# Kernel tuning notes

Hardware: AMD Instinct MI355X
Metric: run time of the kernel (lower is better)

The kernel has to match this reference:

```python
import jax, jax.numpy as jnp
import numpy as np

C_IN, K_R, K_C, N_K = 32, 3, 3, 64
STRIDE = (1, 1)
PAD = (1, 1)


def setup_inputs() -> dict:
    key = jax.random.key(0)
    k1, k2, k3 = jax.random.split(key, 3)
    x = jax.random.normal(k1, (32, C_IN, 128, 128), dtype=jnp.float32)
    kernels = jax.random.normal(k2, (N_K, K_R * K_C * C_IN), dtype=jnp.float32) * 0.05
    bias = jax.random.normal(k3, (N_K, 1), dtype=jnp.float32) * 0.05
    return {"x": x, "kernels": kernels, "bias": bias}


def reference(x, kernels, bias):
    # kernels rows are [C, kr, kc] flattened (per-channel im2col blocks stacked
    # along dim 0 in the original unroll) -> OIHW conv weight.
    w = kernels.reshape(N_K, C_IN, K_R, K_C)
    out = jax.lax.conv_general_dilated(
        x, w,
        window_strides=STRIDE,
        padding=[(PAD[0], PAD[0]), (PAD[1], PAD[1])],
        dimension_numbers=("NCHW", "OIHW", "NCHW"),
    )
    # bias (K, 1) broadcast over all output positions
    return out + bias.reshape(1, N_K, 1, 1)
```

## Files before the change

### kernel.cpp

```cpp
#include <hip/hip_runtime.h>
#include <hip/hip_bf16.h>


typedef __attribute__((ext_vector_type(8))) short bf16x8;
typedef __attribute__((ext_vector_type(4))) float f32x4;

#define NB 32
#define CIN 32
#define HH 128
#define WW 128
#define NK 64
#define XROW (130 * 32)

__device__ __forceinline__ unsigned short f2bf(float f) {
    union { float f; unsigned int u; } v; v.f = f;
    unsigned int u = v.u;
    return (unsigned short)((u + 0x7FFFu + ((u >> 16) & 1u)) >> 16);
}

__device__ __forceinline__ int xel(int wi, int c) {
    return wi * 32 + ((((c >> 3) ^ ((wi >> 2) & 3)) << 3) | (c & 7));
}

__global__ void repack_w(const float* __restrict__ kern,
                         unsigned short* __restrict__ wfrag) {
    int u = blockIdx.x * 256 + threadIdx.x;
    int j = u & 7;
    int lane = (u >> 3) & 63;
    int tile = (u >> 9) & 3;
    int kidx = u >> 11;
    int ok = tile * 16 + (lane & 15);
    int c = ((lane >> 4) << 3) + j;
    wfrag[u] = f2bf(kern[ok * 288 + c * 9 + kidx]);
}

__global__ __launch_bounds__(512, 6) void conv3x3_mfma(
        const float* __restrict__ x, const unsigned short* __restrict__ wfrag,
        const float* __restrict__ bias, float* __restrict__ out) {
    __shared__ unsigned short lds_x[4 * XROW];

    const int tid = threadIdx.x;
    const int bx = blockIdx.x;
    const int hp = ((bx & 7) << 3) | (bx >> 3);
    const int h0 = hp * 2;
    const int n = blockIdx.y;
    const int lane = tid & 63;
    const int l16 = lane & 15;
    const int q = lane >> 4;
    const int wav = tid >> 6;
    const int hsel = wav >> 2;
    const int sub = wav & 3;
    const int ok_tile = (sub & 1) * 2;
    const int w_base = (sub >> 1) * 64;

    if (tid < 256) {
        int it = tid >> 6;
        int idx = tid & 63;
        int c = idx & 31;
        int wi = (idx < 32) ? 0 : 129;
        lds_x[it * XROW + xel(wi, c)] = 0;
    }

    {
        const int c = (tid >> 5) * 2;
        const int wq = tid & 31;
        #pragma unroll
        for (int it = 0; it < 4; ++it) {
            const int r = h0 - 1 + it;
            const bool valid = (unsigned)r < HH;
            float4 va = {0.f, 0.f, 0.f, 0.f}, vb = {0.f, 0.f, 0.f, 0.f};
            if (valid) {
                const float* xrow = x + (((size_t)n * CIN + c) * HH + r) * WW;
                va = *((const float4*)xrow + wq);
                vb = *((const float4*)(xrow + (size_t)HH * WW) + wq);
            }
            unsigned short* lrow = lds_x + it * XROW;
            #pragma unroll
            for (int j = 0; j < 4; ++j) {
                int w = wq * 4 + j;
                __hip_bfloat162 h2 = __float22bfloat162_rn(
                    make_float2((&va.x)[j], (&vb.x)[j]));
                *(unsigned int*)&lrow[xel(w + 1, c)] = *(unsigned int*)&h2;
            }
        }
    }
    __syncthreads();

    f32x4 acc[2][4];
    #pragma unroll
    for (int mi = 0; mi < 2; ++mi)
        #pragma unroll
        for (int ni = 0; ni < 4; ++ni)
            acc[mi][ni] = (f32x4){0.f, 0.f, 0.f, 0.f};

    #pragma unroll 1
    for (int kr = 0; kr < 3; ++kr) {
        const unsigned short* lrow = lds_x + (hsel + kr) * XROW;
        #pragma unroll
        for (int kc = 0; kc < 3; ++kc) {
            const int kidx = kr * 3 + kc;
            bf16x8 afr[2];
            #pragma unroll
            for (int mi = 0; mi < 2; ++mi)
                afr[mi] = *(const bf16x8*)
                    &wfrag[(size_t)(((kidx * 4) + ok_tile + mi) * 64 + lane) * 8];
            #pragma unroll
            for (int ni = 0; ni < 4; ++ni) {
                bf16x8 bfr = *(const bf16x8*)&lrow[xel(w_base + ni * 16 + l16 + kc, q * 8)];
                #pragma unroll
                for (int mi = 0; mi < 2; ++mi)
                    acc[mi][ni] = __builtin_amdgcn_mfma_f32_16x16x32_bf16(
                        afr[mi], bfr, acc[mi][ni], 0, 0, 0);
            }
        }
    }

    const int h = h0 + hsel;
    #pragma unroll
    for (int mi = 0; mi < 2; ++mi) {
        #pragma unroll
        for (int rg = 0; rg < 4; ++rg) {
            int ok = (sub & 1) * 32 + mi * 16 + q * 4 + rg;
            float bv = bias[ok];
            float* orow = out + (((size_t)n * NK + ok) * HH + h) * WW;
            #pragma unroll
            for (int ni = 0; ni < 4; ++ni)
                orow[w_base + ni * 16 + l16] = acc[mi][ni][rg] + bv;
        }
    }
}

extern "C" void kernel_launch(void* const* d_in, const int* in_sizes, int n_in,
                              void* d_out, int out_size, void* d_ws, size_t ws_size,
                              hipStream_t stream) {
    const float* x    = (const float*)d_in[0];
    const float* kern = (const float*)d_in[1];
    const float* bias = (const float*)d_in[2];
    float* out = (float*)d_out;
    unsigned short* wfrag = (unsigned short*)d_ws;

    repack_w<<<72, 256, 0, stream>>>(kern, wfrag);
    dim3 grid(64, NB);
    conv3x3_mfma<<<grid, 512, 0, stream>>>(x, wfrag, bias, out);
}
```

Baseline: 199.6 us.

## Process four output rows per block and prefetch the extra input rows during compute

Each block now produces four output rows in two passes instead of two, with a grid half as large. This reuses the halo rows already staged in LDS and cuts redundant input loads. The two extra input rows are loaded into registers before the first pass and written to LDS afterwards, so their global latency overlaps the first pass's MFMA work. LDS use rises to six rows and the occupancy hint drops to 4, so fewer blocks may be resident.

```diff
diff --git a/kernel.cpp b/kernel.cpp
--- a/kernel.cpp
+++ b/kernel.cpp
@@ -34,15 +34,15 @@
     wfrag[u] = f2bf(kern[ok * 288 + c * 9 + kidx]);
 }
 
-__global__ __launch_bounds__(512, 6) void conv3x3_mfma(
+__global__ __launch_bounds__(512, 4) void conv3x3_mfma(
         const float* __restrict__ x, const unsigned short* __restrict__ wfrag,
         const float* __restrict__ bias, float* __restrict__ out) {
-    __shared__ unsigned short lds_x[4 * XROW];
+    __shared__ unsigned short lds_x[6 * XROW];
 
     const int tid = threadIdx.x;
     const int bx = blockIdx.x;
-    const int hp = ((bx & 7) << 3) | (bx >> 3);
-    const int h0 = hp * 2;
+    const int hgroup = ((bx & 7) << 2) | (bx >> 3);
+    const int h0 = hgroup * 4;
     const int n = blockIdx.y;
     const int lane = tid & 63;
     const int l16 = lane & 15;
@@ -53,7 +53,7 @@
     const int ok_tile = (sub & 1) * 2;
     const int w_base = (sub >> 1) * 64;
 
-    if (tid < 256) {
+    if (tid < 384) {
         int it = tid >> 6;
         int idx = tid & 63;
         int c = idx & 31;
@@ -61,37 +61,48 @@
         lds_x[it * XROW + xel(wi, c)] = 0;
     }
 
-    {
-        const int c = (tid >> 5) * 2;
-        const int wq = tid & 31;
-        #pragma unroll
-        for (int it = 0; it < 4; ++it) {
-            const int r = h0 - 1 + it;
-            const bool valid = (unsigned)r < HH;
-            float4 va = {0.f, 0.f, 0.f, 0.f}, vb = {0.f, 0.f, 0.f, 0.f};
-            if (valid) {
-                const float* xrow = x + (((size_t)n * CIN + c) * HH + r) * WW;
-                va = *((const float4*)xrow + wq);
-                vb = *((const float4*)(xrow + (size_t)HH * WW) + wq);
-            }
-            unsigned short* lrow = lds_x + it * XROW;
-            #pragma unroll
-            for (int j = 0; j < 4; ++j) {
-                int w = wq * 4 + j;
-                __hip_bfloat162 h2 = __float22bfloat162_rn(
-                    make_float2((&va.x)[j], (&vb.x)[j]));
-                *(unsigned int*)&lrow[xel(w + 1, c)] = *(unsigned int*)&h2;
-            }
+    const int c = (tid >> 5) * 2;
+    const int wq = tid & 31;
+
+    #pragma unroll
+    for (int it = 0; it < 4; ++it) {
+        const int r = h0 - 1 + it;
+        const bool valid = (unsigned)r < HH;
+        float4 va = {0.f, 0.f, 0.f, 0.f}, vb = {0.f, 0.f, 0.f, 0.f};
+        if (valid) {
+            const float* xrow = x + (((size_t)n * CIN + c) * HH + r) * WW;
+            va = *((const float4*)xrow + wq);
+            vb = *((const float4*)(xrow + (size_t)HH * WW) + wq);
+        }
+        unsigned short* lrow = lds_x + it * XROW;
+        #pragma unroll
+        for (int j = 0; j < 4; ++j) {
+            int w = wq * 4 + j;
+            __hip_bfloat162 h2 = __float22bfloat162_rn(
+                make_float2((&va.x)[j], (&vb.x)[j]));
+            *(unsigned int*)&lrow[xel(w + 1, c)] = *(unsigned int*)&h2;
+        }
+    }
+
+    float4 p0a, p0b, p1a = {0.f,0.f,0.f,0.f}, p1b = {0.f,0.f,0.f,0.f};
+    {
+        const float* xr3 = x + (((size_t)n * CIN + c) * HH + (h0 + 3)) * WW;
+        p0a = *((const float4*)xr3 + wq);
+        p0b = *((const float4*)(xr3 + (size_t)HH * WW) + wq);
+        if (h0 + 4 < HH) {
+            const float* xr4 = x + (((size_t)n * CIN + c) * HH + (h0 + 4)) * WW;
+            p1a = *((const float4*)xr4 + wq);
+            p1b = *((const float4*)(xr4 + (size_t)HH * WW) + wq);
         }
     }
     __syncthreads();
 
-    f32x4 acc[2][4];
+    f32x4 acc0[2][4];
     #pragma unroll
     for (int mi = 0; mi < 2; ++mi)
         #pragma unroll
         for (int ni = 0; ni < 4; ++ni)
-            acc[mi][ni] = (f32x4){0.f, 0.f, 0.f, 0.f};
+            acc0[mi][ni] = (f32x4){0.f, 0.f, 0.f, 0.f};
 
     #pragma unroll 1
     for (int kr = 0; kr < 3; ++kr) {
@@ -109,23 +120,86 @@
                 bf16x8 bfr = *(const bf16x8*)&lrow[xel(w_base + ni * 16 + l16 + kc, q * 8)];
                 #pragma unroll
                 for (int mi = 0; mi < 2; ++mi)
-                    acc[mi][ni] = __builtin_amdgcn_mfma_f32_16x16x32_bf16(
-                        afr[mi], bfr, acc[mi][ni], 0, 0, 0);
-            }
-        }
-    }
-
-    const int h = h0 + hsel;
+                    acc0[mi][ni] = __builtin_amdgcn_mfma_f32_16x16x32_bf16(
+                        afr[mi], bfr, acc0[mi][ni], 0, 0, 0);
+            }
+        }
+    }
+
+    {
+        unsigned short* l4 = lds_x + 4 * XROW;
+        unsigned short* l5 = lds_x + 5 * XROW;
+        #pragma unroll
+        for (int j = 0; j < 4; ++j) {
+            int w = wq * 4 + j;
+            __hip_bfloat162 h2a = __float22bfloat162_rn(
+                make_float2((&p0a.x)[j], (&p0b.x)[j]));
+            *(unsigned int*)&l4[xel(w + 1, c)] = *(unsigned int*)&h2a;
+            __hip_bfloat162 h2b = __float22bfloat162_rn(
+                make_float2((&p1a.x)[j], (&p1b.x)[j]));
+            *(unsigned int*)&l5[xel(w + 1, c)] = *(unsigned int*)&h2b;
+        }
+    }
+    __syncthreads();
+
+    {
+        const int h = h0 + hsel;
+        #pragma unroll
+        for (int mi = 0; mi < 2; ++mi) {
+            #pragma unroll
+            for (int rg = 0; rg < 4; ++rg) {
+                int ok = (sub & 1) * 32 + mi * 16 + q * 4 + rg;
+                float bv = bias[ok];
+                float* orow = out + (((size_t)n * NK + ok) * HH + h) * WW;
+                #pragma unroll
+                for (int ni = 0; ni < 4; ++ni)
+                    orow[w_base + ni * 16 + l16] = acc0[mi][ni][rg] + bv;
+            }
+        }
+    }
+
+    f32x4 acc1[2][4];
     #pragma unroll
-    for (int mi = 0; mi < 2; ++mi) {
-        #pragma unroll
-        for (int rg = 0; rg < 4; ++rg) {
-            int ok = (sub & 1) * 32 + mi * 16 + q * 4 + rg;
-            float bv = bias[ok];
-            float* orow = out + (((size_t)n * NK + ok) * HH + h) * WW;
-            #pragma unroll
-            for (int ni = 0; ni < 4; ++ni)
-                orow[w_base + ni * 16 + l16] = acc[mi][ni][rg] + bv;
+    for (int mi = 0; mi < 2; ++mi)
+        #pragma unroll
+        for (int ni = 0; ni < 4; ++ni)
+            acc1[mi][ni] = (f32x4){0.f, 0.f, 0.f, 0.f};
+
+    #pragma unroll 1
+    for (int kr = 0; kr < 3; ++kr) {
+        const unsigned short* lrow = lds_x + (2 + hsel + kr) * XROW;
+        #pragma unroll
+        for (int kc = 0; kc < 3; ++kc) {
+            const int kidx = kr * 3 + kc;
+            bf16x8 afr[2];
+            #pragma unroll
+            for (int mi = 0; mi < 2; ++mi)
+                afr[mi] = *(const bf16x8*)
+                    &wfrag[(size_t)(((kidx * 4) + ok_tile + mi) * 64 + lane) * 8];
+            #pragma unroll
+            for (int ni = 0; ni < 4; ++ni) {
+                bf16x8 bfr = *(const bf16x8*)&lrow[xel(w_base + ni * 16 + l16 + kc, q * 8)];
+                #pragma unroll
+                for (int mi = 0; mi < 2; ++mi)
+                    acc1[mi][ni] = __builtin_amdgcn_mfma_f32_16x16x32_bf16(
+                        afr[mi], bfr, acc1[mi][ni], 0, 0, 0);
+            }
+        }
+    }
+
+    {
+        const int h = h0 + 2 + hsel;
+        #pragma unroll
+        for (int mi = 0; mi < 2; ++mi) {
+            #pragma unroll
+            for (int rg = 0; rg < 4; ++rg) {
+                int ok = (sub & 1) * 32 + mi * 16 + q * 4 + rg;
+                float bv = bias[ok];
+                float* orow = out + (((size_t)n * NK + ok) * HH + h) * WW;
+                #pragma unroll
+                for (int ni = 0; ni < 4; ++ni)
+                    orow[w_base + ni * 16 + l16] = acc1[mi][ni][rg] + bv;
+            }
         }
     }
 }
@@ -140,6 +214,6 @@
     unsigned short* wfrag = (unsigned short*)d_ws;
 
     repack_w<<<72, 256, 0, stream>>>(kern, wfrag);
-    dim3 grid(64, NB);
+    dim3 grid(32, NB);
     conv3x3_mfma<<<grid, 512, 0, stream>>>(x, wfrag, bias, out);
 }
```

New measurement: 192.9 us. 1.03x faster.
